# Optimization experiments

Hardware: AMD Instinct MI355X
Metric: run time of the kernel (lower is better)

## Reference

```python
import jax, jax.numpy as jnp
import numpy as np

D, H, CTX, FFN, KS = 512, 8, 128, 2048, 31
B, S = 4, 4096
EPS = 1e-5

def _ln(x, g, b):
    m = jnp.mean(x, -1, keepdims=True)
    v = jnp.mean((x - m) ** 2, -1, keepdims=True)
    return (x - m) * jax.lax.rsqrt(v + EPS) * g + b

def _ffn(x, g, b, w1, b1, w2, b2):
    h = jax.nn.gelu(_ln(x, g, b) @ w1 + b1, approximate=False)
    return h @ w2 + b2

def _local_attn(x, wq, bq, wk, bk, wv, bv, wo, bo, rel_bias):
    Bz, Sz, Dz = x.shape
    Hd = Dz // H
    def proj(w, bias):
        return (x @ w + bias).reshape(Bz, Sz, H, Hd).transpose(0, 2, 1, 3)
    q, k, v = proj(wq, bq), proj(wk, bk), proj(wv, bv)
    nb = Sz // CTX
    def win(t):  # gather 3 neighboring blocks per query block -> [B,H,nb,3*CTX,Hd]
        tp = jnp.pad(t, ((0, 0), (0, 0), (CTX, CTX), (0, 0)))
        tb = tp.reshape(Bz, H, nb + 2, CTX, Hd)
        return jnp.concatenate([tb[:, :, :-2], tb[:, :, 1:-1], tb[:, :, 2:]], axis=3)
    kw, vw = win(k), win(v)
    qb = q.reshape(Bz, H, nb, CTX, Hd)
    scores = jnp.einsum('bhnqd,bhnkd->bhnqk', qb, kw) * (Hd ** -0.5)
    qi = jnp.arange(CTX)[:, None]
    kj = jnp.arange(3 * CTX)[None, :]
    rel = kj - CTX - qi  # [CTX, 3*CTX], relative position j - i
    scores = scores + rel_bias[:, jnp.clip(rel + CTX, 0, 2 * CTX)][None, :, None]
    j_glob = jnp.arange(nb)[:, None, None] * CTX - CTX + kj[None]  # [nb,1,3*CTX]
    valid = (jnp.abs(rel) <= CTX)[None] & (j_glob >= 0) & (j_glob < Sz)  # [nb,CTX,3*CTX]
    scores = jnp.where(valid[None, None], scores, -jnp.inf)
    w = jax.nn.softmax(scores, axis=-1)
    out = jnp.einsum('bhnqk,bhnkd->bhnqd', w, vw).reshape(Bz, H, Sz, Hd)
    out = out.transpose(0, 2, 1, 3).reshape(Bz, Sz, Dz)
    return out @ wo + bo

def _conv_mod(x, g, b, pw1_w, pw1_b, dw_w, dw_b, bn_g, bn_b, bn_m, bn_v, pw2_w, pw2_b):
    h = _ln(x, g, b) @ pw1_w + pw1_b  # [B,S,2D]
    a, gate = jnp.split(h, 2, axis=-1)
    h = a * jax.nn.sigmoid(gate)  # GLU
    hc = h.transpose(0, 2, 1)  # [B,D,S]
    hc = jax.lax.conv_general_dilated(
        hc, dw_w, (1,), [(KS // 2, KS // 2)],
        feature_group_count=D, dimension_numbers=('NCH', 'OIH', 'NCH')) + dw_b[None, :, None]
    hc = (hc - bn_m[None, :, None]) * jax.lax.rsqrt(bn_v[None, :, None] + EPS) * bn_g[None, :, None] + bn_b[None, :, None]
    hc = hc * jax.nn.sigmoid(hc)  # SiLU
    return hc.transpose(0, 2, 1) @ pw2_w + pw2_b

def setup_inputs() -> dict:
    key = jax.random.key(0)
    ks = iter(jax.random.split(key, 40))
    def w(*shape, s=0.02):
        return jax.random.normal(next(ks), shape, dtype=jnp.float32) * s
    d = {}
    d['x'] = jax.random.normal(next(ks), (B, S, D), dtype=jnp.float32)
    for p in ('ff1', 'ff2'):
        d[p + '_ln_g'] = jnp.ones((D,)); d[p + '_ln_b'] = jnp.zeros((D,))
        d[p + '_w1'] = w(D, FFN); d[p + '_b1'] = jnp.zeros((FFN,))
        d[p + '_w2'] = w(FFN, D); d[p + '_b2'] = jnp.zeros((D,))
    d['attn_ln_g'] = jnp.ones((D,)); d['attn_ln_b'] = jnp.zeros((D,))
    for p in ('wq', 'wk', 'wv', 'wo'):
        d[p] = w(D, D)
    for p in ('bq', 'bk', 'bv', 'bo'):
        d[p] = jnp.zeros((D,))
    d['rel_bias'] = w(H, 2 * CTX + 1)
    d['conv_ln_g'] = jnp.ones((D,)); d['conv_ln_b'] = jnp.zeros((D,))
    d['pw1_w'] = w(D, 2 * D); d['pw1_b'] = jnp.zeros((2 * D,))
    d['dw_w'] = w(D, 1, KS); d['dw_b'] = jnp.zeros((D,))
    d['bn_g'] = jnp.ones((D,)); d['bn_b'] = jnp.zeros((D,))
    d['bn_m'] = jnp.zeros((D,)); d['bn_v'] = jnp.ones((D,))
    d['pw2_w'] = w(D, D); d['pw2_b'] = jnp.zeros((D,))
    d['fin_ln_g'] = jnp.ones((D,)); d['fin_ln_b'] = jnp.zeros((D,))
    return d

def reference(x, ff1_ln_g, ff1_ln_b, ff1_w1, ff1_b1, ff1_w2, ff1_b2,
              ff2_ln_g, ff2_ln_b, ff2_w1, ff2_b1, ff2_w2, ff2_b2,
              attn_ln_g, attn_ln_b, wq, wk, wv, wo, bq, bk, bv, bo, rel_bias,
              conv_ln_g, conv_ln_b, pw1_w, pw1_b, dw_w, dw_b,
              bn_g, bn_b, bn_m, bn_v, pw2_w, pw2_b, fin_ln_g, fin_ln_b):
    x = x + 0.5 * _ffn(x, ff1_ln_g, ff1_ln_b, ff1_w1, ff1_b1, ff1_w2, ff1_b2)
    x = x + _local_attn(_ln(x, attn_ln_g, attn_ln_b), wq, bq, wk, bk, wv, bv, wo, bo, rel_bias)
    x = x + _conv_mod(x, conv_ln_g, conv_ln_b, pw1_w, pw1_b, dw_w, dw_b,
                      bn_g, bn_b, bn_m, bn_v, pw2_w, pw2_b)
    x = x + 0.5 * _ffn(x, ff2_ln_g, ff2_ln_b, ff2_w1, ff2_b1, ff2_w2, ff2_b2)
    return _ln(x, fin_ln_g, fin_ln_b)
```

## Files before the change

### kernel.cpp

```cpp
#include <hip/hip_runtime.h>
#include <hip/hip_bf16.h>
#include <math.h>


using bf16 = __hip_bfloat16;
typedef __bf16 bf16x8_t __attribute__((ext_vector_type(8)));
typedef float f32x4_t __attribute__((ext_vector_type(4)));

static __device__ __forceinline__ float bf2f(bf16 v) { return __bfloat162float(v); }
static __device__ __forceinline__ bf16 f2bf(float v) { return __float2bfloat16(v); }

#define GLOAD_LDS16(g, l)                                                            \
    __builtin_amdgcn_global_load_lds((const __attribute__((address_space(1))) void*)(g), \
                                     (__attribute__((address_space(3))) void*)(l), 16, 0, 0)

struct WSrcs { const float* s[10]; };
__global__ __launch_bounds__(256) void k_wconv(WSrcs srcs, bf16* __restrict__ wc) {
    const int start[11] = {0, 1024, 2048, 3072, 4096, 4352, 4608, 4864, 5120, 5632, 5888};
    const int Ks[10]    = {512, 2048, 512, 2048, 512, 512, 512, 512, 512, 512};
    const int Ns[10]    = {2048, 512, 2048, 512, 512, 512, 512, 512, 1024, 512};
    const int doff[10]  = {0, 1048576, 2097152, 3145728, 4194304, 4456448, 4718592, 4980736, 5242880, 5767168};
    int id = blockIdx.x, seg = 0;
#pragma unroll
    for (int i = 1; i < 10; ++i) seg += (id >= start[i]);
    int lid = id - start[seg];
    int K = Ks[seg], N = Ns[seg];
    int nbx = N >> 5;
    int bx = lid % nbx, by = lid / nbx;
    int nb = bx * 32, kb = by * 32;
    const float* in = srcs.s[seg];
    bf16* out = wc + doff[seg];
    bool inter = (seg == 8);
    __shared__ float t[32][33];
    int c = threadIdx.x & 31, r0 = threadIdx.x >> 5;
#pragma unroll
    for (int i = 0; i < 4; ++i)
        t[r0 + i * 8][c] = in[(size_t)(kb + r0 + i * 8) * N + nb + c];
    __syncthreads();
#pragma unroll
    for (int i = 0; i < 4; ++i) {
        int n = nb + r0 + i * 8;
        int orow = inter ? ((n < 512) ? 2 * n : 2 * (n - 512) + 1) : n;
        out[(size_t)orow * K + kb + c] = f2bf(t[c][r0 + i * 8]);
    }
}

template <bool BF16OUT>
__global__ __launch_bounds__(256) void k_ln(const float* __restrict__ x, const float* __restrict__ g,
                                            const float* __restrict__ b, void* __restrict__ outp) {
    int row = blockIdx.x * 4 + (threadIdx.x >> 6), t = threadIdx.x & 63;
    const float* xr = x + (size_t)row * 512 + t * 8;
    float4 v0 = *(const float4*)xr;
    float4 v1 = *(const float4*)(xr + 4);
    float vals[8] = {v0.x, v0.y, v0.z, v0.w, v1.x, v1.y, v1.z, v1.w};
    float s = 0.f, ss = 0.f;
#pragma unroll
    for (int j = 0; j < 8; ++j) { s += vals[j]; ss += vals[j] * vals[j]; }
#pragma unroll
    for (int o = 32; o > 0; o >>= 1) { s += __shfl_xor(s, o, 64); ss += __shfl_xor(ss, o, 64); }
    float mean = s * (1.0f / 512.0f);
    float var  = ss * (1.0f / 512.0f) - mean * mean;
    float r = rsqrtf(var + 1e-5f);
    float4 g0 = *(const float4*)(g + t * 8);
    float4 g1 = *(const float4*)(g + t * 8 + 4);
    float4 b0 = *(const float4*)(b + t * 8);
    float4 b1 = *(const float4*)(b + t * 8 + 4);
    float gv[8] = {g0.x, g0.y, g0.z, g0.w, g1.x, g1.y, g1.z, g1.w};
    float bv[8] = {b0.x, b0.y, b0.z, b0.w, b1.x, b1.y, b1.z, b1.w};
    float ov[8];
#pragma unroll
    for (int j = 0; j < 8; ++j) ov[j] = (vals[j] - mean) * r * gv[j] + bv[j];
    if (BF16OUT) {
        union { uint4 u; bf16 h[8]; } oo;
#pragma unroll
        for (int j = 0; j < 8; ++j) oo.h[j] = f2bf(ov[j]);
        *(uint4*)((bf16*)outp + (size_t)row * 512 + t * 8) = oo.u;
    } else {
        float* op = (float*)outp + (size_t)row * 512 + t * 8;
        *(float4*)op = make_float4(ov[0], ov[1], ov[2], ov[3]);
        *(float4*)(op + 4) = make_float4(ov[4], ov[5], ov[6], ov[7]);
    }
}

template <int MODE, int TN>
__global__ __launch_bounds__(256) void k_gemm(const bf16* __restrict__ A, const bf16* __restrict__ Bt,
                                              const float* __restrict__ bias, void* __restrict__ outp,
                                              int M, int N, int K, float scale,
                                              const float* __restrict__ b2, const float* __restrict__ b3,
                                              const float* __restrict__ resid, int nbx) {
    constexpr int NT = TN / 32;
    __shared__ __align__(16) bf16 As[2][128 * 32];
    __shared__ __align__(16) bf16 Bs[2][TN * 32];
    int id = blockIdx.x;
    int xcd = id & 7, slot = id >> 3;
    int nbyg = (gridDim.x / nbx) >> 3;
    int bxi = slot % nbx;
    int byi = slot / nbx + xcd * nbyg;
    int bn = bxi * TN, bm = byi * 128;
    int tid = threadIdx.x, w = tid >> 6, l = tid & 63;
    int l15 = l & 15, quad = l >> 4;
    int wm = (w >> 1) * 64, wn = (w & 1) * (TN / 2);
    f32x4_t acc[4][NT] = {};
    const int brows = TN / 4;
    const bf16* ag = A + (size_t)(bm + w * 32 + (l >> 2)) * K + (l & 3) * 8;
    const bf16* bg = Bt + (size_t)(bn + w * brows + (l >> 2)) * K + (l & 3) * 8;

    auto stage = [&](int buf, int k0) {
        bf16* asl = As[buf] + w * 32 * 32;
        bf16* bsl = Bs[buf] + w * brows * 32;
#pragma unroll
        for (int j = 0; j < 2; ++j)
            GLOAD_LDS16(ag + (size_t)j * 16 * K + k0, asl + j * 16 * 32);
#pragma unroll
        for (int j = 0; j < TN / 64; ++j)
            GLOAD_LDS16(bg + (size_t)j * 16 * K + k0, bsl + j * 16 * 32);
    };

    const int nt = K >> 5;
    stage(0, 0);
    int cur = 0;
    for (int t = 0; t < nt; ++t) {
        __syncthreads();
        if (t + 1 < nt) stage(cur ^ 1, (t + 1) * 32);
        bf16x8_t af[4], bfr[NT];
#pragma unroll
        for (int tm = 0; tm < 4; ++tm)
            af[tm] = *(const bf16x8_t*)(As[cur] + (wm + tm * 16 + l15) * 32 + quad * 8);
#pragma unroll
        for (int tn = 0; tn < NT; ++tn)
            bfr[tn] = *(const bf16x8_t*)(Bs[cur] + (wn + tn * 16 + l15) * 32 + quad * 8);
#pragma unroll
        for (int tm = 0; tm < 4; ++tm)
#pragma unroll
            for (int tn = 0; tn < NT; ++tn)
                acc[tm][tn] = __builtin_amdgcn_mfma_f32_16x16x32_bf16(af[tm], bfr[tn], acc[tm][tn], 0, 0, 0);
        cur ^= 1;
    }
    __syncthreads();
    float* tb = (float*)(&As[0][0]) + w * 576;
#pragma unroll
    for (int tm = 0; tm < 4; ++tm)
#pragma unroll
        for (int cp = 0; cp < NT / 2; ++cp) {
#pragma unroll
            for (int j = 0; j < 2; ++j)
#pragma unroll
                for (int r = 0; r < 4; ++r)
                    tb[(quad * 4 + r) * 36 + j * 16 + l15] = acc[tm][2 * cp + j][r];
            int lr = l >> 2, lc = (l & 3) * 8;
            float v[8];
#pragma unroll
            for (int i = 0; i < 8; ++i) v[i] = tb[lr * 36 + lc + i];
            int gr = bm + wm + tm * 16 + lr;
            int gc = bn + wn + cp * 32 + lc;
            if (MODE == 0 || MODE == 1) {
                union { uint4 u; bf16 h[8]; } oo;
#pragma unroll
                for (int i = 0; i < 8; ++i) {
                    float vv = v[i] + bias[gc + i];
                    if (MODE == 1) {
                        float z = vv * (1.5957691f + 0.07135481f * vv * vv);
                        vv = vv / (1.f + __expf(-z));
                    }
                    oo.h[i] = f2bf(vv);
                }
                *(uint4*)((bf16*)outp + (size_t)gr * N + gc) = oo.u;
            } else if (MODE == 2) {
                size_t ix = (size_t)gr * N + gc;
                float4 r0 = *(const float4*)(resid + ix);
                float4 r1 = *(const float4*)(resid + ix + 4);
                float rr[8] = {r0.x, r0.y, r0.z, r0.w, r1.x, r1.y, r1.z, r1.w};
                float o[8];
#pragma unroll
                for (int i = 0; i < 8; ++i) o[i] = rr[i] + scale * (v[i] + bias[gc + i]);
                *(float4*)((float*)outp + ix) = make_float4(o[0], o[1], o[2], o[3]);
                *(float4*)((float*)outp + ix + 4) = make_float4(o[4], o[5], o[6], o[7]);
            } else if (MODE == 3) {
                const float* bp = (gc < 512) ? bias : (gc < 1024 ? b2 : b3);
                int cc = gc & 511;
                union { uint4 u; bf16 h[8]; } oo;
#pragma unroll
                for (int i = 0; i < 8; ++i) oo.h[i] = f2bf(v[i] + bp[cc + i]);
                bf16* ob = (bf16*)outp + (size_t)(gc >> 9) * 8388608;
                *(uint4*)(ob + (size_t)gr * 512 + cc) = oo.u;
            } else {
                union { ushort4 u; bf16 h[4]; } oo;
#pragma unroll
                for (int p = 0; p < 4; ++p) {
                    int ic = gc + 2 * p;
                    float a = v[2 * p] + bias[ic >> 1];
                    float gt = v[2 * p + 1] + bias[(ic >> 1) + 512];
                    oo.h[p] = f2bf(a / (1.f + __expf(-gt)));
                }
                *(ushort4*)((bf16*)outp + (size_t)gr * (N >> 1) + (gc >> 1)) = oo.u;
            }
        }
}

__global__ __launch_bounds__(256) void k_attn(const bf16* __restrict__ q, const bf16* __restrict__ k,
                                              const bf16* __restrict__ v, const float* __restrict__ rel_bias,
                                              bf16* __restrict__ out) {
    __shared__ __align__(16) bf16 Ks[64][72];
    __shared__ __align__(16) bf16 Vt[64][72];
    __shared__ __align__(16) bf16 Pb[4][32][72];
    __shared__ float relb[257];
    int blk = blockIdx.x;
    int n = blk & 31, h = (blk >> 5) & 7, b = blk >> 8;
    int tid = threadIdx.x, w = tid >> 6, lane = tid & 63;
    int l15 = lane & 15, quad = lane >> 4;
    for (int i = tid; i < 257; i += 256) relb[i] = rel_bias[h * 257 + i];
    bf16x8_t qf[2][2];
#pragma unroll
    for (int qt = 0; qt < 2; ++qt)
#pragma unroll
        for (int ks = 0; ks < 2; ++ks) {
            const bf16* qg = q + (size_t)(b * 4096 + n * 128 + w * 32 + qt * 16 + l15) * 512
                               + h * 64 + ks * 32 + quad * 8;
            bf16x8_t f = *(const bf16x8_t*)qg;
#pragma unroll
            for (int j = 0; j < 8; ++j) f[j] = (__bf16)(0.125f * (float)f[j]);
            qf[qt][ks] = f;
        }
    float m_run[2][4], l_run[2][4];
#pragma unroll
    for (int qt = 0; qt < 2; ++qt)
#pragma unroll
        for (int r = 0; r < 4; ++r) { m_run[qt][r] = -1e30f; l_run[qt][r] = 0.f; }
    f32x4_t Oacc[2][4] = {};
    int kv0 = n * 128 - 128;
    int lo = (n == 0) ? 2 : 0;
    int hi = (n == 31) ? 4 : 6;
    int krow = tid >> 3, kcol = (tid & 7) * 8;
    int vkey = tid >> 2, vc0 = (tid & 3) * 16;
    uint4 kr0, kr1;
    union { uint4 u[2]; bf16 hh[16]; } vr;
    auto loadKV = [&](int kst) {
        const bf16* kg = k + (size_t)(b * 4096 + kst + krow) * 512 + h * 64 + kcol;
        kr0 = *(const uint4*)kg;
        kr1 = *(const uint4*)(kg + (size_t)32 * 512);
        const bf16* vg = v + (size_t)(b * 4096 + kst + vkey) * 512 + h * 64 + vc0;
        vr.u[0] = *(const uint4*)vg;
        vr.u[1] = *(const uint4*)(vg + 8);
    };
    loadKV(kv0 + lo * 64);
    for (int ch = lo; ch < hi; ++ch) {
        __syncthreads();
        *(uint4*)&Ks[krow][kcol] = kr0;
        *(uint4*)&Ks[krow + 32][kcol] = kr1;
#pragma unroll
        for (int j = 0; j < 16; ++j) Vt[vc0 + j][vkey] = vr.hh[j];
        if (ch + 1 < hi) loadKV(kv0 + (ch + 1) * 64);
        __syncthreads();
        float sc[2][4][4];
#pragma unroll
        for (int qt = 0; qt < 2; ++qt)
#pragma unroll
            for (int nt = 0; nt < 4; ++nt) {
                f32x4_t a = {};
#pragma unroll
                for (int ks = 0; ks < 2; ++ks) {
                    bf16x8_t kf = *(const bf16x8_t*)&Ks[nt * 16 + l15][ks * 32 + quad * 8];
                    a = __builtin_amdgcn_mfma_f32_16x16x32_bf16(qf[qt][ks], kf, a, 0, 0, 0);
                }
#pragma unroll
                for (int r = 0; r < 4; ++r) sc[qt][nt][r] = a[r];
            }
#pragma unroll
        for (int qt = 0; qt < 2; ++qt)
#pragma unroll
            for (int nt = 0; nt < 4; ++nt)
#pragma unroll
                for (int r = 0; r < 4; ++r) {
                    int qrow = w * 32 + qt * 16 + quad * 4 + r;
                    int rel = ch * 64 + nt * 16 + l15 - 128 - qrow;
                    int idx = rel + 128; idx = idx < 0 ? 0 : (idx > 256 ? 256 : idx);
                    float s = sc[qt][nt][r] + relb[idx];
                    sc[qt][nt][r] = (rel >= -128 && rel <= 128) ? s : -INFINITY;
                }
        float al[2][4];
#pragma unroll
        for (int qt = 0; qt < 2; ++qt)
#pragma unroll
            for (int r = 0; r < 4; ++r) {
                float mx = fmaxf(fmaxf(sc[qt][0][r], sc[qt][1][r]), fmaxf(sc[qt][2][r], sc[qt][3][r]));
#pragma unroll
                for (int mk = 1; mk <= 8; mk <<= 1) mx = fmaxf(mx, __shfl_xor(mx, mk, 64));
                float mn = fmaxf(m_run[qt][r], mx);
                float a = __expf(m_run[qt][r] - mn);
                float ps = 0.f;
#pragma unroll
                for (int nt = 0; nt < 4; ++nt) {
                    float p = __expf(sc[qt][nt][r] - mn);
                    sc[qt][nt][r] = p;
                    ps += p;
                }
#pragma unroll
                for (int mk = 1; mk <= 8; mk <<= 1) ps += __shfl_xor(ps, mk, 64);
                l_run[qt][r] = l_run[qt][r] * a + ps;
                m_run[qt][r] = mn;
                al[qt][r] = a;
            }
#pragma unroll
        for (int qt = 0; qt < 2; ++qt)
#pragma unroll
            for (int nt = 0; nt < 4; ++nt)
#pragma unroll
                for (int r = 0; r < 4; ++r)
                    Pb[w][qt * 16 + quad * 4 + r][nt * 16 + l15] = f2bf(sc[qt][nt][r]);
#pragma unroll
        for (int qt = 0; qt < 2; ++qt) {
#pragma unroll
            for (int dt = 0; dt < 4; ++dt)
#pragma unroll
                for (int r = 0; r < 4; ++r)
                    Oacc[qt][dt][r] *= al[qt][r];
            bf16x8_t pf[2];
#pragma unroll
            for (int ks = 0; ks < 2; ++ks)
                pf[ks] = *(const bf16x8_t*)&Pb[w][qt * 16 + l15][ks * 32 + quad * 8];
#pragma unroll
            for (int dt = 0; dt < 4; ++dt) {
                f32x4_t a = Oacc[qt][dt];
#pragma unroll
                for (int ks = 0; ks < 2; ++ks) {
                    bf16x8_t vf = *(const bf16x8_t*)&Vt[dt * 16 + l15][ks * 32 + quad * 8];
                    a = __builtin_amdgcn_mfma_f32_16x16x32_bf16(pf[ks], vf, a, 0, 0, 0);
                }
                Oacc[qt][dt] = a;
            }
        }
    }
#pragma unroll
    for (int qt = 0; qt < 2; ++qt)
#pragma unroll
        for (int r = 0; r < 4; ++r) {
            float inv = 1.f / l_run[qt][r];
            int row = n * 128 + w * 32 + qt * 16 + quad * 4 + r;
#pragma unroll
            for (int dt = 0; dt < 4; ++dt)
                out[(size_t)(b * 4096 + row) * 512 + h * 64 + dt * 16 + l15] = f2bf(Oacc[qt][dt][r] * inv);
        }
}

__global__ __launch_bounds__(256) void k_conv(const bf16* __restrict__ in, const float* __restrict__ w,
                                              const float* __restrict__ wb, const float* __restrict__ bg,
                                              const float* __restrict__ bb2, const float* __restrict__ bm,
                                              const float* __restrict__ bvv, bf16* __restrict__ out) {
    __shared__ float wl[64 * 31];
    int d0 = blockIdx.x * 64, s0 = blockIdx.y * 64, b = blockIdx.z;
    for (int i = threadIdx.x; i < 64 * 31; i += 256) wl[i] = w[d0 * 31 + i];
    __syncthreads();
    int dl = threadIdx.x & 63, chunk = threadIdx.x >> 6;
    int d = d0 + dl;
    int s00 = s0 + chunk * 16;
    float wr[31];
#pragma unroll
    for (int t = 0; t < 31; ++t) wr[t] = wl[dl * 31 + t];
    float xw[46];
    const bf16* base = in + (size_t)(b * 4096) * 512 + d;
#pragma unroll
    for (int i = 0; i < 46; ++i) {
        int s = s00 - 15 + i;
        xw[i] = (s >= 0 && s < 4096) ? bf2f(base[(size_t)s * 512]) : 0.f;
    }
    float scv = bg[d] * rsqrtf(bvv[d] + 1e-5f);
    float wbd = wb[d], bmd = bm[d], bbd = bb2[d];
    bf16* op = out + (size_t)(b * 4096 + s00) * 512 + d;
#pragma unroll
    for (int j = 0; j < 16; ++j) {
        float acc = 0.f;
#pragma unroll
        for (int t = 0; t < 31; ++t) acc += wr[t] * xw[j + t];
        acc += wbd;
        acc = (acc - bmd) * scv + bbd;
        acc = acc / (1.f + __expf(-acc));
        op[(size_t)j * 512] = f2bf(acc);
    }
}

extern "C" void kernel_launch(void* const* d_in, const int* in_sizes, int n_in,
                              void* d_out, int out_size, void* d_ws, size_t ws_size,
                              hipStream_t stream) {
    (void)in_sizes; (void)n_in; (void)out_size; (void)ws_size;
    const float* x = (const float*)d_in[0];
    char* ws = (char*)d_ws;
    float* xf   = (float*)ws;
    bf16* ln_bf = (bf16*)(ws + 33554432);
    bf16* h_bf  = (bf16*)(ws + 50331648);
    bf16* g_bf  = (bf16*)(ws + 117440512);
    bf16* t_bf  = (bf16*)(ws + 134217728);
    bf16* wc    = (bf16*)(ws + 150994944);
    bf16 *qb = h_bf;
    bf16* w_f11 = wc;
    bf16* w_f12 = wc + 1048576;
    bf16* w_f21 = wc + 2097152;
    bf16* w_f22 = wc + 3145728;
    bf16* w_q   = wc + 4194304;
    bf16* w_o   = wc + 4980736;
    bf16* w_p1  = wc + 5242880;
    bf16* w_p2  = wc + 5767168;

    WSrcs srcs;
    srcs.s[0] = (const float*)d_in[3];  srcs.s[1] = (const float*)d_in[5];
    srcs.s[2] = (const float*)d_in[9];  srcs.s[3] = (const float*)d_in[11];
    srcs.s[4] = (const float*)d_in[15]; srcs.s[5] = (const float*)d_in[16];
    srcs.s[6] = (const float*)d_in[17]; srcs.s[7] = (const float*)d_in[18];
    srcs.s[8] = (const float*)d_in[26]; srcs.s[9] = (const float*)d_in[34];
    k_wconv<<<5888, 256, 0, stream>>>(srcs, wc);

    k_ln<true><<<4096, 256, 0, stream>>>(x, (const float*)d_in[1], (const float*)d_in[2], ln_bf);
    k_gemm<1, 128><<<2048, 256, 0, stream>>>(ln_bf, w_f11, (const float*)d_in[4], h_bf, 16384, 2048, 512, 0.f, nullptr, nullptr, nullptr, 16);
    k_gemm<2, 64><<<1024, 256, 0, stream>>>(h_bf, w_f12, (const float*)d_in[6], xf, 16384, 512, 2048, 0.5f, nullptr, nullptr, x, 8);
    k_ln<true><<<4096, 256, 0, stream>>>(xf, (const float*)d_in[13], (const float*)d_in[14], ln_bf);
    k_gemm<3, 64><<<3072, 256, 0, stream>>>(ln_bf, w_q, (const float*)d_in[19], qb, 16384, 1536, 512, 0.f,
                                            (const float*)d_in[20], (const float*)d_in[21], nullptr, 24);
    k_attn<<<1024, 256, 0, stream>>>(qb, qb + 8388608, qb + 16777216, (const float*)d_in[23], t_bf);
    k_gemm<2, 64><<<1024, 256, 0, stream>>>(t_bf, w_o, (const float*)d_in[22], xf, 16384, 512, 512, 1.0f, nullptr, nullptr, xf, 8);
    k_ln<true><<<4096, 256, 0, stream>>>(xf, (const float*)d_in[24], (const float*)d_in[25], ln_bf);
    k_gemm<5, 64><<<2048, 256, 0, stream>>>(ln_bf, w_p1, (const float*)d_in[27], g_bf, 16384, 1024, 512, 0.f, nullptr, nullptr, nullptr, 16);
    k_conv<<<dim3(8, 64, 4), 256, 0, stream>>>(g_bf, (const float*)d_in[28], (const float*)d_in[29], (const float*)d_in[30],
                                               (const float*)d_in[31], (const float*)d_in[32], (const float*)d_in[33], t_bf);
    k_gemm<2, 64><<<1024, 256, 0, stream>>>(t_bf, w_p2, (const float*)d_in[35], xf, 16384, 512, 512, 1.0f, nullptr, nullptr, xf, 8);
    k_ln<true><<<4096, 256, 0, stream>>>(xf, (const float*)d_in[7], (const float*)d_in[8], ln_bf);
    k_gemm<1, 128><<<2048, 256, 0, stream>>>(ln_bf, w_f21, (const float*)d_in[10], h_bf, 16384, 2048, 512, 0.f, nullptr, nullptr, nullptr, 16);
    k_gemm<2, 64><<<1024, 256, 0, stream>>>(h_bf, w_f22, (const float*)d_in[12], xf, 16384, 512, 2048, 0.5f, nullptr, nullptr, xf, 8);
    k_ln<false><<<4096, 256, 0, stream>>>(xf, (const float*)d_in[36], (const float*)d_in[37], d_out);
}
```

Before: 640.9 us.

## Precompute masked rel-bias table, add lazy softmax rescale, and MFMA priority hints

The attention kernel now builds a 512-entry shared table holding the relative-position bias with -inf already in place for out-of-window offsets. This removes the per-element clamp, mask compare and select from the score loop. It also adds a lazy online-softmax rescale: the running max and the output accumulator are only updated when some row's new max exceeds the old one by more than 8, checked wave-wide with __any. s_setprio hints are placed around the MFMA blocks. The lazy rescale lets unnormalised exponentials grow up to e^8, which is a small numerical risk in bf16/fp32, and the first chunk always takes the slow path.

```diff
diff --git a/kernel.cpp b/kernel.cpp
--- a/kernel.cpp
+++ b/kernel.cpp
@@ -203,12 +203,15 @@
     __shared__ __align__(16) bf16 Ks[64][72];
     __shared__ __align__(16) bf16 Vt[64][72];
     __shared__ __align__(16) bf16 Pb[4][32][72];
-    __shared__ float relb[257];
+    __shared__ float relb2[512];
     int blk = blockIdx.x;
     int n = blk & 31, h = (blk >> 5) & 7, b = blk >> 8;
     int tid = threadIdx.x, w = tid >> 6, lane = tid & 63;
     int l15 = lane & 15, quad = lane >> 4;
-    for (int i = tid; i < 257; i += 256) relb[i] = rel_bias[h * 257 + i];
+    for (int i = tid; i < 512; i += 256) {
+        int rel = i - 255;
+        relb2[i] = (rel >= -128 && rel <= 128) ? rel_bias[h * 257 + rel + 128] : -INFINITY;
+    }
     bf16x8_t qf[2][2];
 #pragma unroll
     for (int qt = 0; qt < 2; ++qt)
@@ -230,6 +233,7 @@
     int kv0 = n * 128 - 128;
     int lo = (n == 0) ? 2 : 0;
     int hi = (n == 31) ? 4 : 6;
+    int tbase = l15 + 127 - w * 32 - quad * 4;
     int krow = tid >> 3, kcol = (tid & 7) * 8;
     int vkey = tid >> 2, vc0 = (tid & 3) * 16;
     uint4 kr0, kr1;
@@ -252,6 +256,7 @@
         if (ch + 1 < hi) loadKV(kv0 + (ch + 1) * 64);
         __syncthreads();
         float sc[2][4][4];
+        __builtin_amdgcn_s_setprio(1);
 #pragma unroll
         for (int qt = 0; qt < 2; ++qt)
 #pragma unroll
@@ -265,28 +270,36 @@
 #pragma unroll
                 for (int r = 0; r < 4; ++r) sc[qt][nt][r] = a[r];
             }
+        __builtin_amdgcn_s_setprio(0);
+        {
+            int tb0 = tbase + ch * 64;
+#pragma unroll
+            for (int qt = 0; qt < 2; ++qt)
+#pragma unroll
+                for (int nt = 0; nt < 4; ++nt)
+#pragma unroll
+                    for (int r = 0; r < 4; ++r)
+                        sc[qt][nt][r] += relb2[tb0 + nt * 16 - qt * 16 - r];
+        }
+        float mx[2][4];
+        int need = 0;
 #pragma unroll
         for (int qt = 0; qt < 2; ++qt)
 #pragma unroll
-            for (int nt = 0; nt < 4; ++nt)
-#pragma unroll
-                for (int r = 0; r < 4; ++r) {
-                    int qrow = w * 32 + qt * 16 + quad * 4 + r;
-                    int rel = ch * 64 + nt * 16 + l15 - 128 - qrow;
-                    int idx = rel + 128; idx = idx < 0 ? 0 : (idx > 256 ? 256 : idx);
-                    float s = sc[qt][nt][r] + relb[idx];
-                    sc[qt][nt][r] = (rel >= -128 && rel <= 128) ? s : -INFINITY;
-                }
+            for (int r = 0; r < 4; ++r) {
+                float m3 = fmaxf(fmaxf(sc[qt][0][r], sc[qt][1][r]), fmaxf(sc[qt][2][r], sc[qt][3][r]));
+#pragma unroll
+                for (int mk = 1; mk <= 8; mk <<= 1) m3 = fmaxf(m3, __shfl_xor(m3, mk, 64));
+                mx[qt][r] = m3;
+                need |= (m3 > m_run[qt][r] + 8.f) ? 1 : 0;
+            }
+        bool slow = __any(need);
         float al[2][4];
 #pragma unroll
         for (int qt = 0; qt < 2; ++qt)
 #pragma unroll
             for (int r = 0; r < 4; ++r) {
-                float mx = fmaxf(fmaxf(sc[qt][0][r], sc[qt][1][r]), fmaxf(sc[qt][2][r], sc[qt][3][r]));
-#pragma unroll
-                for (int mk = 1; mk <= 8; mk <<= 1) mx = fmaxf(mx, __shfl_xor(mx, mk, 64));
-                float mn = fmaxf(m_run[qt][r], mx);
-                float a = __expf(m_run[qt][r] - mn);
+                float mn = slow ? fmaxf(m_run[qt][r], mx[qt][r]) : m_run[qt][r];
                 float ps = 0.f;
 #pragma unroll
                 for (int nt = 0; nt < 4; ++nt) {
@@ -296,9 +309,14 @@
                 }
 #pragma unroll
                 for (int mk = 1; mk <= 8; mk <<= 1) ps += __shfl_xor(ps, mk, 64);
-                l_run[qt][r] = l_run[qt][r] * a + ps;
-                m_run[qt][r] = mn;
-                al[qt][r] = a;
+                if (slow) {
+                    float a = __expf(m_run[qt][r] - mn);
+                    l_run[qt][r] = l_run[qt][r] * a + ps;
+                    m_run[qt][r] = mn;
+                    al[qt][r] = a;
+                } else {
+                    l_run[qt][r] += ps;
+                }
             }
 #pragma unroll
         for (int qt = 0; qt < 2; ++qt)
@@ -309,15 +327,18 @@
                     Pb[w][qt * 16 + quad * 4 + r][nt * 16 + l15] = f2bf(sc[qt][nt][r]);
 #pragma unroll
         for (int qt = 0; qt < 2; ++qt) {
-#pragma unroll
-            for (int dt = 0; dt < 4; ++dt)
-#pragma unroll
-                for (int r = 0; r < 4; ++r)
-                    Oacc[qt][dt][r] *= al[qt][r];
+            if (slow) {
+#pragma unroll
+                for (int dt = 0; dt < 4; ++dt)
+#pragma unroll
+                    for (int r = 0; r < 4; ++r)
+                        Oacc[qt][dt][r] *= al[qt][r];
+            }
             bf16x8_t pf[2];
 #pragma unroll
             for (int ks = 0; ks < 2; ++ks)
                 pf[ks] = *(const bf16x8_t*)&Pb[w][qt * 16 + l15][ks * 32 + quad * 8];
+            __builtin_amdgcn_s_setprio(1);
 #pragma unroll
             for (int dt = 0; dt < 4; ++dt) {
                 f32x4_t a = Oacc[qt][dt];
@@ -328,6 +349,7 @@
                 }
                 Oacc[qt][dt] = a;
             }
+            __builtin_amdgcn_s_setprio(0);
         }
     }
 #pragma unroll
```

Measured after the change: 627.2 us. 2.1% less time.
